# Kernel tuning notes

Measured on AMD Instinct MI355X. Metric: run time of the kernel, lower is better.

## Reference

```python
import jax, jax.numpy as jnp
import numpy as np

N = 50000      # nodes
E = 800000     # edges
DN = 128       # input node feature dim
D = 64         # dim_embed
H = 2          # attention heads (layer 0)
NEG_SLOPE = 0.2
LN_EPS = 1e-5


def setup_inputs() -> dict:
    key = jax.random.key(0)
    ks = jax.random.split(key, 10)
    s = 0.1  # weight scale
    return {
        "h":  jax.random.normal(ks[0], (N, DN), jnp.float32),
        "W0": jax.random.normal(ks[1], (DN, H * D), jnp.float32) * s,
        "al0": jax.random.normal(ks[2], (H, D), jnp.float32) * s,
        "ar0": jax.random.normal(ks[3], (H, D), jnp.float32) * s,
        "b0": jnp.zeros((H * D,), jnp.float32),
        "W1": jax.random.normal(ks[4], (H * D, D), jnp.float32) * s,
        "al1": jax.random.normal(ks[5], (1, D), jnp.float32) * s,
        "ar1": jax.random.normal(ks[6], (1, D), jnp.float32) * s,
        "b1": jnp.zeros((D,), jnp.float32),
        "g0": jnp.ones((H * D,), jnp.float32),
        "be0": jnp.zeros((H * D,), jnp.float32),
        "g1": jnp.ones((D,), jnp.float32),
        "be1": jnp.zeros((D,), jnp.float32),
        "src": jax.random.randint(ks[7], (E,), 0, N, jnp.int32),
        "dst": jax.random.randint(ks[8], (E,), 0, N, jnp.int32),
    }


def layer_norm(x, g, b):
    mu = jnp.mean(x, axis=-1, keepdims=True)
    var = jnp.mean(jnp.square(x - mu), axis=-1, keepdims=True)
    return (x - mu) * jax.lax.rsqrt(var + LN_EPS) * g + b


def gat_conv(h, W, attn_l, attn_r, bias, src, dst, heads, dim):
    # DGL GATConv (feat_drop=attn_drop=0, allow_zero_in_degree=True, bias=True)
    feat = (h @ W).reshape(-1, heads, dim)            # [N, H, D]
    el = jnp.einsum("nhd,hd->nh", feat, attn_l)       # [N, H]
    er = jnp.einsum("nhd,hd->nh", feat, attn_r)       # [N, H]
    e = jax.nn.leaky_relu(el[src] + er[dst], NEG_SLOPE)  # [E, H]
    # segment softmax over incoming edges of each dst node
    m = jax.ops.segment_max(e, dst, num_segments=N)      # [N, H]
    p = jnp.exp(e - m[dst])                              # [E, H]
    denom = jax.ops.segment_sum(p, dst, num_segments=N)  # [N, H]
    alpha = p / denom[dst]                               # [E, H]
    msg = feat[src] * alpha[:, :, None]                  # [E, H, D]
    rst = jax.ops.segment_sum(msg, dst, num_segments=N)  # [N, H, D]
    return rst + bias.reshape(1, heads, dim)


def reference(h, W0, al0, ar0, b0, W1, al1, ar1, b1, g0, be0, g1, be1, src, dst):
    # layer 0: H heads, relu(flatten), layer norm
    x = gat_conv(h, W0, al0, ar0, b0, src, dst, H, D)     # [N, H, D]
    x = jax.nn.relu(x.reshape(N, H * D))
    x = layer_norm(x, g0, be0)
    # layer 1: 1 head, mean over heads (== squeeze), layer norm
    y = gat_conv(x, W1, al1, ar1, b1, src, dst, 1, D)     # [N, 1, D]
    y = jnp.mean(y, axis=1)                               # [N, D]
    return layer_norm(y, g1, be1)
```

## Files before the change

kernel.cpp:

```cpp
#include <hip/hip_runtime.h>
#include <hip/hip_bf16.h>


#define NN 50000
#define EE 800000
#define NBUCK 196
#define CHUNK 4096
#define CAP 8192
#define GB0 ((NN + 63) / 64)

typedef _Float16 h2 __attribute__((ext_vector_type(2)));
typedef _Float16 h4 __attribute__((ext_vector_type(4)));
typedef _Float16 h8 __attribute__((ext_vector_type(8)));
typedef float f32x4 __attribute__((ext_vector_type(4)));

__device__ __forceinline__ h2 i2h(int v) { union { int i; h2 h; } u; u.i = v; return u.h; }
__device__ __forceinline__ int h2i(h2 v) { union { h2 h; int i; } u; u.h = v; return u.i; }

#define SEL_LO 0x01000504u
#define SEL_HI 0x03020706u

__global__ __launch_bounds__(1024) void k_bin(
    const int* __restrict__ src, const int* __restrict__ dst,
    int* __restrict__ bcntp, unsigned int* __restrict__ staging,
    const float* __restrict__ W0, const float* __restrict__ W1,
    h8* __restrict__ Wp0, h8* __restrict__ Wp1)
{
    int tid = threadIdx.x;
    if (blockIdx.x >= (EE + CHUNK - 1) / CHUNK) {
        int idx = (blockIdx.x - (EE + CHUNK - 1) / CHUNK) * 1024 + tid;
        if (idx < 2048) {
            int lane = idx & 63, kk = (idx >> 6) & 3, tt = idx >> 8;
            int q = lane >> 4, c = lane & 15;
            h8 v;
#pragma unroll
            for (int j = 0; j < 8; ++j)
                v[j] = (_Float16)W0[(kk * 32 + q * 8 + j) * 128 + tt * 16 + c];
            Wp0[idx] = v;
        } else if (idx < 3072) {
            int i2_ = idx - 2048;
            int lane = i2_ & 63, kk = (i2_ >> 6) & 3, tt = i2_ >> 8;
            int q = lane >> 4, c = lane & 15;
            h8 v;
#pragma unroll
            for (int j = 0; j < 8; ++j)
                v[j] = (_Float16)W1[(kk * 32 + q * 8 + j) * 64 + tt * 16 + c];
            Wp1[i2_] = v;
        }
        return;
    }
    __shared__ int hist[NBUCK];
    __shared__ int rnk[NBUCK];
    __shared__ int gbase[NBUCK];
    int base = blockIdx.x * CHUNK;
    int m = EE - base; if (m > CHUNK) m = CHUNK;
    if (tid < NBUCK) { hist[tid] = 0; rnk[tid] = 0; }
    __syncthreads();
    int e0 = tid * 4;
    bool act = e0 < m;
    int4 d4 = {0, 0, 0, 0}, s4 = {0, 0, 0, 0};
    if (act) {
        d4 = ((const int4*)(dst + base))[tid];
        s4 = ((const int4*)(src + base))[tid];
        atomicAdd(&hist[d4.x >> 8], 1);
        atomicAdd(&hist[d4.y >> 8], 1);
        atomicAdd(&hist[d4.z >> 8], 1);
        atomicAdd(&hist[d4.w >> 8], 1);
    }
    __syncthreads();
    if (tid < NBUCK && hist[tid])
        gbase[tid] = atomicAdd(&bcntp[tid * 16], hist[tid]);
    __syncthreads();
    if (act) {
        int d[4] = {d4.x, d4.y, d4.z, d4.w};
        int s[4] = {s4.x, s4.y, s4.z, s4.w};
#pragma unroll
        for (int k = 0; k < 4; ++k) {
            int b = d[k] >> 8;
            int r = atomicAdd(&rnk[b], 1);
            int slot = gbase[b] + r;
            if (slot < CAP)
                staging[(size_t)b * CAP + slot] =
                    ((unsigned)(d[k] & 255) << 16) | (unsigned)s[k];
        }
    }
}

#define HS_STRIDE 136
#define D0_STRIDE 132
__global__ __launch_bounds__(256) void k_gemm0(
    const float* __restrict__ h, const h8* __restrict__ Wp0,
    const float* __restrict__ al0, const float* __restrict__ ar0,
    _Float16* __restrict__ feat0, float* __restrict__ el0, float* __restrict__ er0,
    const int* __restrict__ bcntp, int* __restrict__ bexc, int* __restrict__ off)
{
    int tid = threadIdx.x;
    __shared__ char smem[64 * D0_STRIDE * 4];
    if (blockIdx.x == GB0) {
        int* s = (int*)smem;
        int v = (tid < NBUCK) ? bcntp[tid * 16] : 0;
        s[tid] = v;
        __syncthreads();
        for (int o = 1; o < 256; o <<= 1) {
            int u = (tid >= o) ? s[tid - o] : 0;
            __syncthreads();
            s[tid] += u;
            __syncthreads();
        }
        if (tid < NBUCK) bexc[tid] = s[tid] - v;
        if (tid == 0) off[0] = 0;
        return;
    }
    _Float16* hs = (_Float16*)smem;
    float* ds2 = (float*)smem;
    int n0 = blockIdx.x * 64;
#pragma unroll
    for (int r = 0; r < 8; ++r) {
        int f = tid + 256 * r;
        int node = f >> 5, kc = f & 31;
        int n = n0 + node;
        float4 v = {0.f, 0.f, 0.f, 0.f};
        if (n < NN) v = ((const float4*)h)[(size_t)n * 32 + kc];
        h4 hv; hv[0] = (_Float16)v.x; hv[1] = (_Float16)v.y;
        hv[2] = (_Float16)v.z; hv[3] = (_Float16)v.w;
        *(h4*)&hs[node * HS_STRIDE + kc * 4] = hv;
    }
    __syncthreads();
    int w = tid >> 6, lane = tid & 63;
    int m = lane & 15, q = lane >> 4;
    h8 aF[4];
#pragma unroll
    for (int kk = 0; kk < 4; ++kk)
        aF[kk] = *(const h8*)&hs[(w * 16 + m) * HS_STRIDE + kk * 32 + q * 8];
    __syncthreads();
#pragma unroll
    for (int t = 0; t < 8; ++t) {
        f32x4 acc = {0.f, 0.f, 0.f, 0.f};
#pragma unroll
        for (int kk = 0; kk < 4; ++kk) {
            h8 bF = Wp0[(t * 4 + kk) * 64 + lane];
            acc = __builtin_amdgcn_mfma_f32_16x16x32_f16(aF[kk], bF, acc, 0, 0, 0);
        }
#pragma unroll
        for (int r = 0; r < 4; ++r)
            ds2[(w * 16 + q * 4 + r) * D0_STRIDE + t * 16 + m] = acc[r];
    }
    __syncthreads();
#pragma unroll
    for (int r = 0; r < 4; ++r) {
        int f = tid + 256 * r;
        int node = f >> 4, c8 = f & 15;
        int n = n0 + node;
        if (n < NN) {
            float4 a = *(const float4*)&ds2[node * D0_STRIDE + c8 * 8];
            float4 b = *(const float4*)&ds2[node * D0_STRIDE + c8 * 8 + 4];
            h8 v;
            v[0] = (_Float16)a.x; v[1] = (_Float16)a.y; v[2] = (_Float16)a.z; v[3] = (_Float16)a.w;
            v[4] = (_Float16)b.x; v[5] = (_Float16)b.y; v[6] = (_Float16)b.z; v[7] = (_Float16)b.w;
            ((h8*)feat0)[(size_t)n * 16 + c8] = v;
        }
    }
    {
        int node = tid >> 2, qq = tid & 3;
        int n = n0 + node;
        float pl = 0.f, pr = 0.f;
#pragma unroll
        for (int i = 0; i < 8; ++i) {
            float4 v = *(const float4*)&ds2[node * D0_STRIDE + qq * 32 + i * 4];
            float4 a = ((const float4*)al0)[qq * 8 + i];
            float4 r = ((const float4*)ar0)[qq * 8 + i];
            pl += v.x * a.x + v.y * a.y + v.z * a.z + v.w * a.w;
            pr += v.x * r.x + v.y * r.y + v.z * r.z + v.w * r.w;
        }
        pl += __shfl_xor(pl, 1, 4); pr += __shfl_xor(pr, 1, 4);
        if (n < NN) {
            if (qq == 0) { el0[n * 2] = pl;     er0[n * 2] = pr; }
            if (qq == 2) { el0[n * 2 + 1] = pl; er0[n * 2 + 1] = pr; }
        }
    }
}

__global__ __launch_bounds__(256) void k_final(
    const unsigned int* __restrict__ staging, const int* __restrict__ bcntp,
    const int* __restrict__ bexc, int* __restrict__ off,
    unsigned short* __restrict__ ssort)
{
    int b = blockIdx.x;
    int tid = threadIdx.x;
    int cnt = bcntp[b * 16]; if (cnt > CAP) cnt = CAP;
    size_t base = (size_t)b * CAP;
    int lo = bexc[b];
    __shared__ unsigned short buf[CAP];
    __shared__ int hist[256];
    __shared__ int sc[256];
    hist[tid] = 0;
    __syncthreads();
    for (int i = tid; i < cnt; i += 256)
        atomicAdd(&hist[staging[base + i] >> 16], 1);
    __syncthreads();
    int hv = hist[tid];
    sc[tid] = hv;
    __syncthreads();
    for (int o = 1; o < 256; o <<= 1) {
        int u = (tid >= o) ? sc[tid - o] : 0;
        __syncthreads();
        sc[tid] += u;
        __syncthreads();
    }
    int nlo = b << 8;
    int nrem = NN - nlo; if (nrem > 256) nrem = 256;
    if (tid < nrem) off[nlo + tid + 1] = lo + sc[tid];
    hist[tid] = sc[tid] - hv;
    __syncthreads();
    for (int i = tid; i < cnt; i += 256) {
        unsigned rec = staging[base + i];
        int r = atomicAdd(&hist[rec >> 16], 1);
        buf[r] = (unsigned short)(rec & 0xFFFFu);
    }
    __syncthreads();
    for (int i = tid; i < cnt; i += 256)
        ssort[lo + i] = buf[i];
}

#define D1_STRIDE 68
__global__ __launch_bounds__(1024) void k_aggemm(
    const int* __restrict__ off, const unsigned short* __restrict__ ssort,
    const float* __restrict__ el0, const float* __restrict__ er0,
    const _Float16* __restrict__ feat0, const float* __restrict__ b0,
    const float* __restrict__ g0, const float* __restrict__ be0,
    const h8* __restrict__ Wp1, const float* __restrict__ al1,
    const float* __restrict__ ar1,
    _Float16* __restrict__ feat1, float* __restrict__ el1, float* __restrict__ er1)
{
    int tid = threadIdx.x;
    int w16 = tid >> 6, lane = tid & 63;
    int grp = lane >> 4, c = lane & 15;
    int n0 = blockIdx.x * 64;
    __shared__ char smem[64 * HS_STRIDE * 2 > 64 * D1_STRIDE * 4
                         ? 64 * HS_STRIDE * 2 : 64 * D1_STRIDE * 4];
    __shared__ int2 esc[16][64];
    _Float16* xs = (_Float16*)smem;
    float* ds2 = (float*)smem;
    const int4* fb = (const int4*)feat0;
    unsigned qsel = (c < 8) ? SEL_LO : SEL_HI;
    for (int i = 0; i < 4; ++i) {
        int nl = w16 * 4 + i;
        int n = n0 + nl;
        if (n < NN) {
            int beg = off[n], end = off[n + 1];
            float2 ern2 = ((const float2*)er0)[n];
            float acc[8] = {};
            float den0 = 0.f, den1 = 0.f;
            for (int cb = beg; cb < end; cb += 64) {
                int m = end - cb; if (m > 64) m = 64;
                int s_reg = 0; float p0 = 0.f, p1 = 0.f;
                if (lane < m) {
                    s_reg = ssort[cb + lane];
                    float2 el2 = ((const float2*)el0)[s_reg];
                    float v0 = el2.x + ern2.x; v0 = v0 > 0.f ? v0 : 0.2f * v0;
                    float v1 = el2.y + ern2.y; v1 = v1 > 0.f ? v1 : 0.2f * v1;
                    p0 = __expf(v0); p1 = __expf(v1);
                }
                den0 += p0; den1 += p1;
                h2 pp; pp[0] = (_Float16)p0; pp[1] = (_Float16)p1;
                esc[w16][lane] = make_int2(s_reg, h2i(pp));
                for (int ii = 0; ii < m; ii += 8) {
                    int4 rr = *(const int4*)&esc[w16][ii + grp * 2];
                    int qp = __builtin_amdgcn_perm(rr.y, rr.w, qsel);
                    int4 iA = fb[(size_t)rr.x * 16 + c];
                    int4 iB = fb[(size_t)rr.z * 16 + c];
                    h2 q2 = i2h(qp);
                    int pe, po;
                    pe = __builtin_amdgcn_perm(iA.x, iB.x, SEL_LO);
                    po = __builtin_amdgcn_perm(iA.x, iB.x, SEL_HI);
                    acc[0] = __builtin_amdgcn_fdot2(i2h(pe), q2, acc[0], false);
                    acc[1] = __builtin_amdgcn_fdot2(i2h(po), q2, acc[1], false);
                    pe = __builtin_amdgcn_perm(iA.y, iB.y, SEL_LO);
                    po = __builtin_amdgcn_perm(iA.y, iB.y, SEL_HI);
                    acc[2] = __builtin_amdgcn_fdot2(i2h(pe), q2, acc[2], false);
                    acc[3] = __builtin_amdgcn_fdot2(i2h(po), q2, acc[3], false);
                    pe = __builtin_amdgcn_perm(iA.z, iB.z, SEL_LO);
                    po = __builtin_amdgcn_perm(iA.z, iB.z, SEL_HI);
                    acc[4] = __builtin_amdgcn_fdot2(i2h(pe), q2, acc[4], false);
                    acc[5] = __builtin_amdgcn_fdot2(i2h(po), q2, acc[5], false);
                    pe = __builtin_amdgcn_perm(iA.w, iB.w, SEL_LO);
                    po = __builtin_amdgcn_perm(iA.w, iB.w, SEL_HI);
                    acc[6] = __builtin_amdgcn_fdot2(i2h(pe), q2, acc[6], false);
                    acc[7] = __builtin_amdgcn_fdot2(i2h(po), q2, acc[7], false);
                }
            }
#pragma unroll
            for (int k = 0; k < 8; ++k) {
                acc[k] += __shfl_down(acc[k], 32);
                acc[k] += __shfl_down(acc[k], 16);
            }
#pragma unroll
            for (int o = 32; o > 0; o >>= 1) { den0 += __shfl_down(den0, o); den1 += __shfl_down(den1, o); }
            den0 = __shfl(den0, 0); den1 = __shfl(den1, 0);
            float den = (c < 8) ? den0 : den1;
            float inv = (end > beg) ? 1.f / den : 0.f;
            float4 ba = ((const float4*)b0)[c * 2];
            float4 bb = ((const float4*)b0)[c * 2 + 1];
            float val[8];
            val[0] = fmaxf(acc[0] * inv + ba.x, 0.f);
            val[1] = fmaxf(acc[1] * inv + ba.y, 0.f);
            val[2] = fmaxf(acc[2] * inv + ba.z, 0.f);
            val[3] = fmaxf(acc[3] * inv + ba.w, 0.f);
            val[4] = fmaxf(acc[4] * inv + bb.x, 0.f);
            val[5] = fmaxf(acc[5] * inv + bb.y, 0.f);
            val[6] = fmaxf(acc[6] * inv + bb.z, 0.f);
            val[7] = fmaxf(acc[7] * inv + bb.w, 0.f);
            float s1 = 0.f, s2 = 0.f;
#pragma unroll
            for (int k = 0; k < 8; ++k) { s1 += val[k]; s2 += val[k] * val[k]; }
#pragma unroll
            for (int o = 1; o < 16; o <<= 1) { s1 += __shfl_xor(s1, o, 16); s2 += __shfl_xor(s2, o, 16); }
            float mu = s1 * (1.f / 128.f);
            float var = s2 * (1.f / 128.f) - mu * mu;
            float rs = rsqrtf(var + 1e-5f);
            if (grp == 0) {
                float4 ga = ((const float4*)g0)[c * 2];
                float4 gb = ((const float4*)g0)[c * 2 + 1];
                float4 ea = ((const float4*)be0)[c * 2];
                float4 eb = ((const float4*)be0)[c * 2 + 1];
                h8 xv;
                xv[0] = (_Float16)((val[0] - mu) * rs * ga.x + ea.x);
                xv[1] = (_Float16)((val[1] - mu) * rs * ga.y + ea.y);
                xv[2] = (_Float16)((val[2] - mu) * rs * ga.z + ea.z);
                xv[3] = (_Float16)((val[3] - mu) * rs * ga.w + ea.w);
                xv[4] = (_Float16)((val[4] - mu) * rs * gb.x + eb.x);
                xv[5] = (_Float16)((val[5] - mu) * rs * gb.y + eb.y);
                xv[6] = (_Float16)((val[6] - mu) * rs * gb.z + eb.z);
                xv[7] = (_Float16)((val[7] - mu) * rs * gb.w + eb.w);
                *(h8*)&xs[nl * HS_STRIDE + c * 8] = xv;
            }
        } else if (grp == 0) {
            h8 z = {};
            *(h8*)&xs[nl * HS_STRIDE + c * 8] = z;
        }
    }
    __syncthreads();
    int rg = w16 & 3, t = w16 >> 2;
    int m = lane & 15, q = lane >> 4;
    h8 aF[4];
#pragma unroll
    for (int kk = 0; kk < 4; ++kk)
        aF[kk] = *(const h8*)&xs[(rg * 16 + m) * HS_STRIDE + kk * 32 + q * 8];
    __syncthreads();
    f32x4 acc1 = {0.f, 0.f, 0.f, 0.f};
#pragma unroll
    for (int kk = 0; kk < 4; ++kk) {
        h8 bF = Wp1[(t * 4 + kk) * 64 + lane];
        acc1 = __builtin_amdgcn_mfma_f32_16x16x32_f16(aF[kk], bF, acc1, 0, 0, 0);
    }
#pragma unroll
    for (int r = 0; r < 4; ++r)
        ds2[(rg * 16 + q * 4 + r) * D1_STRIDE + t * 16 + m] = acc1[r];
    __syncthreads();
    if (tid < 512) {
        int node = tid >> 3, c8 = tid & 7;
        int n = n0 + node;
        if (n < NN) {
            float4 a = *(const float4*)&ds2[node * D1_STRIDE + c8 * 8];
            float4 b = *(const float4*)&ds2[node * D1_STRIDE + c8 * 8 + 4];
            h8 v;
            v[0] = (_Float16)a.x; v[1] = (_Float16)a.y; v[2] = (_Float16)a.z; v[3] = (_Float16)a.w;
            v[4] = (_Float16)b.x; v[5] = (_Float16)b.y; v[6] = (_Float16)b.z; v[7] = (_Float16)b.w;
            ((h8*)feat1)[(size_t)n * 8 + c8] = v;
        }
    } else if (tid < 768) {
        int t2 = tid - 512;
        int node = t2 >> 2, qq = t2 & 3;
        int n = n0 + node;
        float pl = 0.f, pr = 0.f;
#pragma unroll
        for (int i = 0; i < 4; ++i) {
            float4 v = *(const float4*)&ds2[node * D1_STRIDE + qq * 16 + i * 4];
            float4 a = ((const float4*)al1)[qq * 4 + i];
            float4 r = ((const float4*)ar1)[qq * 4 + i];
            pl += v.x * a.x + v.y * a.y + v.z * a.z + v.w * a.w;
            pr += v.x * r.x + v.y * r.y + v.z * r.z + v.w * r.w;
        }
        pl += __shfl_xor(pl, 1, 4); pr += __shfl_xor(pr, 1, 4);
        pl += __shfl_xor(pl, 2, 4); pr += __shfl_xor(pr, 2, 4);
        if (qq == 0 && n < NN) { el1[n] = pl; er1[n] = pr; }
    }
}

__global__ __launch_bounds__(256) void k_agg1(
    const int* __restrict__ off, const unsigned short* __restrict__ ssort,
    const float* __restrict__ el1, const float* __restrict__ er1,
    const _Float16* __restrict__ feat1, const float* __restrict__ b1,
    const float* __restrict__ g1, const float* __restrict__ be1,
    float* __restrict__ out)
{
    int w = threadIdx.x >> 6, lane = threadIdx.x & 63;
    int grp = lane >> 3, c = lane & 7;
    int n = blockIdx.x * 4 + w;
    int beg = off[n], end = off[n + 1];
    float ern = er1[n];
    const int4* fb = (const int4*)feat1;
    __shared__ int2 esc[4][64];
    float acc[8] = {};
    float den = 0.f;
    for (int cb = beg; cb < end; cb += 64) {
        int m = end - cb; if (m > 64) m = 64;
        int s_reg = 0; float p_reg = 0.f;
        if (lane < m) {
            s_reg = ssort[cb + lane];
            float v = el1[s_reg] + ern;
            v = v > 0.f ? v : 0.2f * v;
            p_reg = __expf(v);
        }
        den += p_reg;
        h2 pp; pp[0] = (_Float16)p_reg; pp[1] = (_Float16)0.f;
        esc[w][lane] = make_int2(s_reg, h2i(pp));
        for (int i = 0; i < m; i += 16) {
            int4 rr = *(const int4*)&esc[w][i + grp * 2];
            int qp = __builtin_amdgcn_perm(rr.y, rr.w, SEL_LO);
            int4 iA = fb[(size_t)rr.x * 8 + c];
            int4 iB = fb[(size_t)rr.z * 8 + c];
            h2 q2 = i2h(qp);
            int pe, po;
            pe = __builtin_amdgcn_perm(iA.x, iB.x, SEL_LO);
            po = __builtin_amdgcn_perm(iA.x, iB.x, SEL_HI);
            acc[0] = __builtin_amdgcn_fdot2(i2h(pe), q2, acc[0], false);
            acc[1] = __builtin_amdgcn_fdot2(i2h(po), q2, acc[1], false);
            pe = __builtin_amdgcn_perm(iA.y, iB.y, SEL_LO);
            po = __builtin_amdgcn_perm(iA.y, iB.y, SEL_HI);
            acc[2] = __builtin_amdgcn_fdot2(i2h(pe), q2, acc[2], false);
            acc[3] = __builtin_amdgcn_fdot2(i2h(po), q2, acc[3], false);
            pe = __builtin_amdgcn_perm(iA.z, iB.z, SEL_LO);
            po = __builtin_amdgcn_perm(iA.z, iB.z, SEL_HI);
            acc[4] = __builtin_amdgcn_fdot2(i2h(pe), q2, acc[4], false);
            acc[5] = __builtin_amdgcn_fdot2(i2h(po), q2, acc[5], false);
            pe = __builtin_amdgcn_perm(iA.w, iB.w, SEL_LO);
            po = __builtin_amdgcn_perm(iA.w, iB.w, SEL_HI);
            acc[6] = __builtin_amdgcn_fdot2(i2h(pe), q2, acc[6], false);
            acc[7] = __builtin_amdgcn_fdot2(i2h(po), q2, acc[7], false);
        }
    }
#pragma unroll
    for (int k = 0; k < 8; ++k) {
        acc[k] += __shfl_down(acc[k], 32);
        acc[k] += __shfl_down(acc[k], 16);
        acc[k] += __shfl_down(acc[k], 8);
    }
#pragma unroll
    for (int o = 32; o > 0; o >>= 1) den += __shfl_down(den, o);
    den = __shfl(den, 0);
    float inv = (end > beg) ? 1.f / den : 0.f;
    float4 ba = ((const float4*)b1)[c * 2];
    float4 bb = ((const float4*)b1)[c * 2 + 1];
    float val[8];
    val[0] = acc[0] * inv + ba.x; val[1] = acc[1] * inv + ba.y;
    val[2] = acc[2] * inv + ba.z; val[3] = acc[3] * inv + ba.w;
    val[4] = acc[4] * inv + bb.x; val[5] = acc[5] * inv + bb.y;
    val[6] = acc[6] * inv + bb.z; val[7] = acc[7] * inv + bb.w;
    float s1 = 0.f, s2 = 0.f;
#pragma unroll
    for (int k = 0; k < 8; ++k) { s1 += val[k]; s2 += val[k] * val[k]; }
#pragma unroll
    for (int o = 1; o < 8; o <<= 1) { s1 += __shfl_xor(s1, o, 8); s2 += __shfl_xor(s2, o, 8); }
    float mu = s1 * (1.f / 64.f);
    float var = s2 * (1.f / 64.f) - mu * mu;
    float rs = rsqrtf(var + 1e-5f);
    if (lane < 8) {
        float4 ga = ((const float4*)g1)[c * 2];
        float4 gb = ((const float4*)g1)[c * 2 + 1];
        float4 ea = ((const float4*)be1)[c * 2];
        float4 eb = ((const float4*)be1)[c * 2 + 1];
        float4 oa, ob;
        oa.x = (val[0] - mu) * rs * ga.x + ea.x;
        oa.y = (val[1] - mu) * rs * ga.y + ea.y;
        oa.z = (val[2] - mu) * rs * ga.z + ea.z;
        oa.w = (val[3] - mu) * rs * ga.w + ea.w;
        ob.x = (val[4] - mu) * rs * gb.x + eb.x;
        ob.y = (val[5] - mu) * rs * gb.y + eb.y;
        ob.z = (val[6] - mu) * rs * gb.z + eb.z;
        ob.w = (val[7] - mu) * rs * gb.w + eb.w;
        float4* orow = (float4*)(out + (size_t)n * 64);
        orow[c * 2] = oa;
        orow[c * 2 + 1] = ob;
    }
}

extern "C" void kernel_launch(void* const* d_in, const int* in_sizes, int n_in,
                              void* d_out, int out_size, void* d_ws, size_t ws_size,
                              hipStream_t stream)
{
    const float* h   = (const float*)d_in[0];
    const float* W0  = (const float*)d_in[1];
    const float* al0 = (const float*)d_in[2];
    const float* ar0 = (const float*)d_in[3];
    const float* b0  = (const float*)d_in[4];
    const float* W1  = (const float*)d_in[5];
    const float* al1 = (const float*)d_in[6];
    const float* ar1 = (const float*)d_in[7];
    const float* b1  = (const float*)d_in[8];
    const float* g0  = (const float*)d_in[9];
    const float* be0 = (const float*)d_in[10];
    const float* g1  = (const float*)d_in[11];
    const float* be1 = (const float*)d_in[12];
    const int*   src = (const int*)d_in[13];
    const int*   dst = (const int*)d_in[14];
    float* out = (float*)d_out;

    char* p = (char*)d_ws;
    auto alloc = [&](size_t bytes) -> char* {
        char* r = p;
        p += (bytes + 255) & ~(size_t)255;
        return r;
    };
    _Float16* feat0 = (_Float16*)alloc((size_t)NN * 128 * sizeof(_Float16));
    float* el0   = (float*)alloc((size_t)NN * 2 * sizeof(float));
    float* er0   = (float*)alloc((size_t)NN * 2 * sizeof(float));
    _Float16* feat1 = (_Float16*)alloc((size_t)NN * 64 * sizeof(_Float16));
    float* el1   = (float*)alloc((size_t)NN * sizeof(float));
    float* er1   = (float*)alloc((size_t)NN * sizeof(float));
    int*   bcntp = (int*)alloc((size_t)NBUCK * 16 * sizeof(int));
    int*   bexc  = (int*)alloc((size_t)NBUCK * sizeof(int));
    int*   off   = (int*)alloc((size_t)(NN + 1) * sizeof(int));
    unsigned int*   staging = (unsigned int*)alloc((size_t)NBUCK * CAP * sizeof(unsigned int));
    unsigned short* ssort   = (unsigned short*)alloc((size_t)EE * sizeof(unsigned short));
    h8*    Wp0   = (h8*)alloc(2048 * sizeof(h8));
    h8*    Wp1   = (h8*)alloc(1024 * sizeof(h8));

    hipMemsetAsync(bcntp, 0, (size_t)NBUCK * 16 * sizeof(int), stream);

    const int NBBIN = (EE + CHUNK - 1) / CHUNK;
    k_bin<<<NBBIN + 3, 1024, 0, stream>>>(src, dst, bcntp, staging, W0, W1, Wp0, Wp1);
    k_gemm0<<<GB0 + 1, 256, 0, stream>>>(h, Wp0, al0, ar0, feat0, el0, er0,
                                         bcntp, bexc, off);
    k_final<<<NBUCK, 256, 0, stream>>>(staging, bcntp, bexc, off, ssort);
    k_aggemm<<<(NN + 63) / 64, 1024, 0, stream>>>(off, ssort, el0, er0, feat0,
                                                  b0, g0, be0, Wp1, al1, ar1,
                                                  feat1, el1, er1);
    k_agg1<<<NN / 4, 256, 0, stream>>>(off, ssort, el1, er1, feat1, b1, g1, be1, out);
}
```

Measured before the change: 208.8 us.

## Fuse binning with layer-0 GEMM, move bucket scan into sort, remap aggregation lanes per node

Replaces the memset and weight-packing prologue with a small init kernel, and merges edge binning with the layer-0 GEMM into one 1024-thread launch. The bucket prefix scan moves into each k_final block, which removes the bexc buffer. Both aggregation kernels now assign one node per 16-lane (layer 0) or 8-lane (layer 1) group instead of one node per wavefront. This drops the cross-lane accumulator reductions and raises occupancy for the low-degree nodes. The cost is redundant scans across blocks and less memory-level parallelism on high-degree nodes.

```diff
diff --git a/kernel.cpp b/kernel.cpp
--- a/kernel.cpp
+++ b/kernel.cpp
@@ -7,7 +7,7 @@
 #define NBUCK 196
 #define CHUNK 4096
 #define CAP 8192
-#define GB0 ((NN + 63) / 64)
+#define NBBIN 196
 
 typedef _Float16 h2 __attribute__((ext_vector_type(2)));
 typedef _Float16 h4 __attribute__((ext_vector_type(4)));
@@ -20,103 +20,90 @@
 #define SEL_LO 0x01000504u
 #define SEL_HI 0x03020706u
 
-__global__ __launch_bounds__(1024) void k_bin(
+__global__ __launch_bounds__(1024) void k_init(
+    const float* __restrict__ W0, const float* __restrict__ W1,
+    h8* __restrict__ Wp0, h8* __restrict__ Wp1, int* __restrict__ bcntp)
+{
+    int tid = threadIdx.x;
+    int b = blockIdx.x;
+    if (b < 2) {
+        int idx = b * 1024 + tid;
+        int lane = idx & 63, kk = (idx >> 6) & 3, tt = idx >> 8;
+        int q = lane >> 4, c = lane & 15;
+        h8 v;
+#pragma unroll
+        for (int j = 0; j < 8; ++j)
+            v[j] = (_Float16)W0[(kk * 32 + q * 8 + j) * 128 + tt * 16 + c];
+        Wp0[idx] = v;
+    } else if (b == 2) {
+        int idx = tid;
+        int lane = idx & 63, kk = (idx >> 6) & 3, tt = idx >> 8;
+        int q = lane >> 4, c = lane & 15;
+        h8 v;
+#pragma unroll
+        for (int j = 0; j < 8; ++j)
+            v[j] = (_Float16)W1[(kk * 32 + q * 8 + j) * 64 + tt * 16 + c];
+        Wp1[idx] = v;
+    } else {
+        for (int i = tid; i < NBUCK * 16; i += 1024) bcntp[i] = 0;
+    }
+}
+
+#define HS_STRIDE 136
+#define D0_STRIDE 132
+__global__ __launch_bounds__(1024) void k_work(
     const int* __restrict__ src, const int* __restrict__ dst,
     int* __restrict__ bcntp, unsigned int* __restrict__ staging,
-    const float* __restrict__ W0, const float* __restrict__ W1,
-    h8* __restrict__ Wp0, h8* __restrict__ Wp1)
+    const float* __restrict__ h, const h8* __restrict__ Wp0,
+    const float* __restrict__ al0, const float* __restrict__ ar0,
+    _Float16* __restrict__ feat0, float* __restrict__ el0, float* __restrict__ er0)
 {
     int tid = threadIdx.x;
-    if (blockIdx.x >= (EE + CHUNK - 1) / CHUNK) {
-        int idx = (blockIdx.x - (EE + CHUNK - 1) / CHUNK) * 1024 + tid;
-        if (idx < 2048) {
-            int lane = idx & 63, kk = (idx >> 6) & 3, tt = idx >> 8;
-            int q = lane >> 4, c = lane & 15;
-            h8 v;
-#pragma unroll
-            for (int j = 0; j < 8; ++j)
-                v[j] = (_Float16)W0[(kk * 32 + q * 8 + j) * 128 + tt * 16 + c];
-            Wp0[idx] = v;
-        } else if (idx < 3072) {
-            int i2_ = idx - 2048;
-            int lane = i2_ & 63, kk = (i2_ >> 6) & 3, tt = i2_ >> 8;
-            int q = lane >> 4, c = lane & 15;
-            h8 v;
-#pragma unroll
-            for (int j = 0; j < 8; ++j)
-                v[j] = (_Float16)W1[(kk * 32 + q * 8 + j) * 64 + tt * 16 + c];
-            Wp1[i2_] = v;
-        }
-        return;
-    }
+    __shared__ char smem[64 * D0_STRIDE * 4];
     __shared__ int hist[NBUCK];
     __shared__ int rnk[NBUCK];
     __shared__ int gbase[NBUCK];
-    int base = blockIdx.x * CHUNK;
-    int m = EE - base; if (m > CHUNK) m = CHUNK;
-    if (tid < NBUCK) { hist[tid] = 0; rnk[tid] = 0; }
-    __syncthreads();
-    int e0 = tid * 4;
-    bool act = e0 < m;
-    int4 d4 = {0, 0, 0, 0}, s4 = {0, 0, 0, 0};
-    if (act) {
-        d4 = ((const int4*)(dst + base))[tid];
-        s4 = ((const int4*)(src + base))[tid];
-        atomicAdd(&hist[d4.x >> 8], 1);
-        atomicAdd(&hist[d4.y >> 8], 1);
-        atomicAdd(&hist[d4.z >> 8], 1);
-        atomicAdd(&hist[d4.w >> 8], 1);
-    }
-    __syncthreads();
-    if (tid < NBUCK && hist[tid])
-        gbase[tid] = atomicAdd(&bcntp[tid * 16], hist[tid]);
-    __syncthreads();
-    if (act) {
-        int d[4] = {d4.x, d4.y, d4.z, d4.w};
-        int s[4] = {s4.x, s4.y, s4.z, s4.w};
-#pragma unroll
-        for (int k = 0; k < 4; ++k) {
-            int b = d[k] >> 8;
-            int r = atomicAdd(&rnk[b], 1);
-            int slot = gbase[b] + r;
-            if (slot < CAP)
-                staging[(size_t)b * CAP + slot] =
-                    ((unsigned)(d[k] & 255) << 16) | (unsigned)s[k];
-        }
-    }
-}
-
-#define HS_STRIDE 136
-#define D0_STRIDE 132
-__global__ __launch_bounds__(256) void k_gemm0(
-    const float* __restrict__ h, const h8* __restrict__ Wp0,
-    const float* __restrict__ al0, const float* __restrict__ ar0,
-    _Float16* __restrict__ feat0, float* __restrict__ el0, float* __restrict__ er0,
-    const int* __restrict__ bcntp, int* __restrict__ bexc, int* __restrict__ off)
-{
-    int tid = threadIdx.x;
-    __shared__ char smem[64 * D0_STRIDE * 4];
-    if (blockIdx.x == GB0) {
-        int* s = (int*)smem;
-        int v = (tid < NBUCK) ? bcntp[tid * 16] : 0;
-        s[tid] = v;
-        __syncthreads();
-        for (int o = 1; o < 256; o <<= 1) {
-            int u = (tid >= o) ? s[tid - o] : 0;
-            __syncthreads();
-            s[tid] += u;
-            __syncthreads();
-        }
-        if (tid < NBUCK) bexc[tid] = s[tid] - v;
-        if (tid == 0) off[0] = 0;
+    if (blockIdx.x < NBBIN) {
+        int base = blockIdx.x * CHUNK;
+        int m = EE - base; if (m > CHUNK) m = CHUNK;
+        if (tid < NBUCK) { hist[tid] = 0; rnk[tid] = 0; }
+        __syncthreads();
+        int e0 = tid * 4;
+        bool act = e0 < m;
+        int4 d4 = {0, 0, 0, 0}, s4 = {0, 0, 0, 0};
+        if (act) {
+            d4 = ((const int4*)(dst + base))[tid];
+            s4 = ((const int4*)(src + base))[tid];
+            atomicAdd(&hist[d4.x >> 8], 1);
+            atomicAdd(&hist[d4.y >> 8], 1);
+            atomicAdd(&hist[d4.z >> 8], 1);
+            atomicAdd(&hist[d4.w >> 8], 1);
+        }
+        __syncthreads();
+        if (tid < NBUCK && hist[tid])
+            gbase[tid] = atomicAdd(&bcntp[tid * 16], hist[tid]);
+        __syncthreads();
+        if (act) {
+            int d[4] = {d4.x, d4.y, d4.z, d4.w};
+            int s[4] = {s4.x, s4.y, s4.z, s4.w};
+#pragma unroll
+            for (int k = 0; k < 4; ++k) {
+                int b = d[k] >> 8;
+                int r = atomicAdd(&rnk[b], 1);
+                int slot = gbase[b] + r;
+                if (slot < CAP)
+                    staging[(size_t)b * CAP + slot] =
+                        ((unsigned)(d[k] & 255) << 16) | (unsigned)s[k];
+            }
+        }
         return;
     }
     _Float16* hs = (_Float16*)smem;
     float* ds2 = (float*)smem;
-    int n0 = blockIdx.x * 64;
-#pragma unroll
-    for (int r = 0; r < 8; ++r) {
-        int f = tid + 256 * r;
+    int n0 = (blockIdx.x - NBBIN) * 64;
+#pragma unroll
+    for (int r = 0; r < 2; ++r) {
+        int f = tid + 1024 * r;
         int node = f >> 5, kc = f & 31;
         int n = n0 + node;
         float4 v = {0.f, 0.f, 0.f, 0.f};
@@ -126,15 +113,17 @@
         *(h4*)&hs[node * HS_STRIDE + kc * 4] = hv;
     }
     __syncthreads();
-    int w = tid >> 6, lane = tid & 63;
+    int w16 = tid >> 6, lane = tid & 63;
+    int rg = w16 & 3, tt = w16 >> 2;
     int m = lane & 15, q = lane >> 4;
     h8 aF[4];
 #pragma unroll
     for (int kk = 0; kk < 4; ++kk)
-        aF[kk] = *(const h8*)&hs[(w * 16 + m) * HS_STRIDE + kk * 32 + q * 8];
-    __syncthreads();
-#pragma unroll
-    for (int t = 0; t < 8; ++t) {
+        aF[kk] = *(const h8*)&hs[(rg * 16 + m) * HS_STRIDE + kk * 32 + q * 8];
+    __syncthreads();
+#pragma unroll
+    for (int t2 = 0; t2 < 2; ++t2) {
+        int t = tt * 2 + t2;
         f32x4 acc = {0.f, 0.f, 0.f, 0.f};
 #pragma unroll
         for (int kk = 0; kk < 4; ++kk) {
@@ -143,13 +132,11 @@
         }
 #pragma unroll
         for (int r = 0; r < 4; ++r)
-            ds2[(w * 16 + q * 4 + r) * D0_STRIDE + t * 16 + m] = acc[r];
-    }
-    __syncthreads();
-#pragma unroll
-    for (int r = 0; r < 4; ++r) {
-        int f = tid + 256 * r;
-        int node = f >> 4, c8 = f & 15;
+            ds2[(rg * 16 + q * 4 + r) * D0_STRIDE + t * 16 + m] = acc[r];
+    }
+    __syncthreads();
+    {
+        int node = tid >> 4, c8 = tid & 15;
         int n = n0 + node;
         if (n < NN) {
             float4 a = *(const float4*)&ds2[node * D0_STRIDE + c8 * 8];
@@ -160,7 +147,7 @@
             ((h8*)feat0)[(size_t)n * 16 + c8] = v;
         }
     }
-    {
+    if (tid < 256) {
         int node = tid >> 2, qq = tid & 3;
         int n = n0 + node;
         float pl = 0.f, pr = 0.f;
@@ -182,17 +169,27 @@
 
 __global__ __launch_bounds__(256) void k_final(
     const unsigned int* __restrict__ staging, const int* __restrict__ bcntp,
-    const int* __restrict__ bexc, int* __restrict__ off,
-    unsigned short* __restrict__ ssort)
+    int* __restrict__ off, unsigned short* __restrict__ ssort)
 {
     int b = blockIdx.x;
     int tid = threadIdx.x;
     int cnt = bcntp[b * 16]; if (cnt > CAP) cnt = CAP;
     size_t base = (size_t)b * CAP;
-    int lo = bexc[b];
     __shared__ unsigned short buf[CAP];
     __shared__ int hist[256];
     __shared__ int sc[256];
+    int bv = (tid < NBUCK) ? bcntp[tid * 16] : 0;
+    sc[tid] = bv;
+    __syncthreads();
+    for (int o = 1; o < 256; o <<= 1) {
+        int u = (tid >= o) ? sc[tid - o] : 0;
+        __syncthreads();
+        sc[tid] += u;
+        __syncthreads();
+    }
+    int lo = (b > 0) ? sc[b - 1] : 0;
+    if (b == 0 && tid == 0) off[0] = 0;
+    __syncthreads();
     hist[tid] = 0;
     __syncthreads();
     for (int i = tid; i < cnt; i += 256)
@@ -234,28 +231,28 @@
 {
     int tid = threadIdx.x;
     int w16 = tid >> 6, lane = tid & 63;
-    int grp = lane >> 4, c = lane & 15;
+    int g = lane >> 4, c = lane & 15;
     int n0 = blockIdx.x * 64;
     __shared__ char smem[64 * HS_STRIDE * 2 > 64 * D1_STRIDE * 4
                          ? 64 * HS_STRIDE * 2 : 64 * D1_STRIDE * 4];
-    __shared__ int2 esc[16][64];
+    __shared__ int2 esc[16][4][18];
     _Float16* xs = (_Float16*)smem;
     float* ds2 = (float*)smem;
     const int4* fb = (const int4*)feat0;
     unsigned qsel = (c < 8) ? SEL_LO : SEL_HI;
-    for (int i = 0; i < 4; ++i) {
-        int nl = w16 * 4 + i;
+    {
+        int nl = w16 * 4 + g;
         int n = n0 + nl;
         if (n < NN) {
             int beg = off[n], end = off[n + 1];
             float2 ern2 = ((const float2*)er0)[n];
             float acc[8] = {};
             float den0 = 0.f, den1 = 0.f;
-            for (int cb = beg; cb < end; cb += 64) {
-                int m = end - cb; if (m > 64) m = 64;
+            for (int cb = beg; cb < end; cb += 16) {
+                int m = end - cb; if (m > 16) m = 16;
                 int s_reg = 0; float p0 = 0.f, p1 = 0.f;
-                if (lane < m) {
-                    s_reg = ssort[cb + lane];
+                if (c < m) {
+                    s_reg = ssort[cb + c];
                     float2 el2 = ((const float2*)el0)[s_reg];
                     float v0 = el2.x + ern2.x; v0 = v0 > 0.f ? v0 : 0.2f * v0;
                     float v1 = el2.y + ern2.y; v1 = v1 > 0.f ? v1 : 0.2f * v1;
@@ -263,9 +260,9 @@
                 }
                 den0 += p0; den1 += p1;
                 h2 pp; pp[0] = (_Float16)p0; pp[1] = (_Float16)p1;
-                esc[w16][lane] = make_int2(s_reg, h2i(pp));
-                for (int ii = 0; ii < m; ii += 8) {
-                    int4 rr = *(const int4*)&esc[w16][ii + grp * 2];
+                esc[w16][g][c] = make_int2(s_reg, h2i(pp));
+                for (int ii = 0; ii < m; ii += 2) {
+                    int4 rr = *(const int4*)&esc[w16][g][ii];
                     int qp = __builtin_amdgcn_perm(rr.y, rr.w, qsel);
                     int4 iA = fb[(size_t)rr.x * 16 + c];
                     int4 iB = fb[(size_t)rr.z * 16 + c];
@@ -290,13 +287,10 @@
                 }
             }
 #pragma unroll
-            for (int k = 0; k < 8; ++k) {
-                acc[k] += __shfl_down(acc[k], 32);
-                acc[k] += __shfl_down(acc[k], 16);
+            for (int o = 1; o < 16; o <<= 1) {
+                den0 += __shfl_xor(den0, o, 16);
+                den1 += __shfl_xor(den1, o, 16);
             }
-#pragma unroll
-            for (int o = 32; o > 0; o >>= 1) { den0 += __shfl_down(den0, o); den1 += __shfl_down(den1, o); }
-            den0 = __shfl(den0, 0); den1 = __shfl(den1, 0);
             float den = (c < 8) ? den0 : den1;
             float inv = (end > beg) ? 1.f / den : 0.f;
             float4 ba = ((const float4*)b0)[c * 2];
@@ -318,23 +312,21 @@
             float mu = s1 * (1.f / 128.f);
             float var = s2 * (1.f / 128.f) - mu * mu;
             float rs = rsqrtf(var + 1e-5f);
-            if (grp == 0) {
-                float4 ga = ((const float4*)g0)[c * 2];
-                float4 gb = ((const float4*)g0)[c * 2 + 1];
-                float4 ea = ((const float4*)be0)[c * 2];
-                float4 eb = ((const float4*)be0)[c * 2 + 1];
-                h8 xv;
-                xv[0] = (_Float16)((val[0] - mu) * rs * ga.x + ea.x);
-                xv[1] = (_Float16)((val[1] - mu) * rs * ga.y + ea.y);
-                xv[2] = (_Float16)((val[2] - mu) * rs * ga.z + ea.z);
-                xv[3] = (_Float16)((val[3] - mu) * rs * ga.w + ea.w);
-                xv[4] = (_Float16)((val[4] - mu) * rs * gb.x + eb.x);
-                xv[5] = (_Float16)((val[5] - mu) * rs * gb.y + eb.y);
-                xv[6] = (_Float16)((val[6] - mu) * rs * gb.z + eb.z);
-                xv[7] = (_Float16)((val[7] - mu) * rs * gb.w + eb.w);
-                *(h8*)&xs[nl * HS_STRIDE + c * 8] = xv;
-            }
-        } else if (grp == 0) {
+            float4 ga = ((const float4*)g0)[c * 2];
+            float4 gb = ((const float4*)g0)[c * 2 + 1];
+            float4 ea = ((const float4*)be0)[c * 2];
+            float4 eb = ((const float4*)be0)[c * 2 + 1];
+            h8 xv;
+            xv[0] = (_Float16)((val[0] - mu) * rs * ga.x + ea.x);
+            xv[1] = (_Float16)((val[1] - mu) * rs * ga.y + ea.y);
+            xv[2] = (_Float16)((val[2] - mu) * rs * ga.z + ea.z);
+            xv[3] = (_Float16)((val[3] - mu) * rs * ga.w + ea.w);
+            xv[4] = (_Float16)((val[4] - mu) * rs * gb.x + eb.x);
+            xv[5] = (_Float16)((val[5] - mu) * rs * gb.y + eb.y);
+            xv[6] = (_Float16)((val[6] - mu) * rs * gb.z + eb.z);
+            xv[7] = (_Float16)((val[7] - mu) * rs * gb.w + eb.w);
+            *(h8*)&xs[nl * HS_STRIDE + c * 8] = xv;
+        } else {
             h8 z = {};
             *(h8*)&xs[nl * HS_STRIDE + c * 8] = z;
         }
@@ -395,28 +387,29 @@
     float* __restrict__ out)
 {
     int w = threadIdx.x >> 6, lane = threadIdx.x & 63;
-    int grp = lane >> 3, c = lane & 7;
-    int n = blockIdx.x * 4 + w;
+    int g = lane >> 3, c = lane & 7;
+    int n = blockIdx.x * 32 + w * 8 + g;
+    __shared__ int2 esc[4][8][10];
+    const int4* fb = (const int4*)feat1;
+    if (n >= NN) return;
     int beg = off[n], end = off[n + 1];
     float ern = er1[n];
-    const int4* fb = (const int4*)feat1;
-    __shared__ int2 esc[4][64];
     float acc[8] = {};
     float den = 0.f;
-    for (int cb = beg; cb < end; cb += 64) {
-        int m = end - cb; if (m > 64) m = 64;
+    for (int cb = beg; cb < end; cb += 8) {
+        int m = end - cb; if (m > 8) m = 8;
         int s_reg = 0; float p_reg = 0.f;
-        if (lane < m) {
-            s_reg = ssort[cb + lane];
+        if (c < m) {
+            s_reg = ssort[cb + c];
             float v = el1[s_reg] + ern;
             v = v > 0.f ? v : 0.2f * v;
             p_reg = __expf(v);
         }
         den += p_reg;
         h2 pp; pp[0] = (_Float16)p_reg; pp[1] = (_Float16)0.f;
-        esc[w][lane] = make_int2(s_reg, h2i(pp));
-        for (int i = 0; i < m; i += 16) {
-            int4 rr = *(const int4*)&esc[w][i + grp * 2];
+        esc[w][g][c] = make_int2(s_reg, h2i(pp));
+        for (int ii = 0; ii < m; ii += 2) {
+            int4 rr = *(const int4*)&esc[w][g][ii];
             int qp = __builtin_amdgcn_perm(rr.y, rr.w, SEL_LO);
             int4 iA = fb[(size_t)rr.x * 8 + c];
             int4 iB = fb[(size_t)rr.z * 8 + c];
@@ -441,14 +434,7 @@
         }
     }
 #pragma unroll
-    for (int k = 0; k < 8; ++k) {
-        acc[k] += __shfl_down(acc[k], 32);
-        acc[k] += __shfl_down(acc[k], 16);
-        acc[k] += __shfl_down(acc[k], 8);
-    }
-#pragma unroll
-    for (int o = 32; o > 0; o >>= 1) den += __shfl_down(den, o);
-    den = __shfl(den, 0);
+    for (int o = 1; o < 8; o <<= 1) den += __shfl_xor(den, o, 8);
     float inv = (end > beg) ? 1.f / den : 0.f;
     float4 ba = ((const float4*)b1)[c * 2];
     float4 bb = ((const float4*)b1)[c * 2 + 1];
@@ -465,24 +451,22 @@
     float mu = s1 * (1.f / 64.f);
     float var = s2 * (1.f / 64.f) - mu * mu;
     float rs = rsqrtf(var + 1e-5f);
-    if (lane < 8) {
-        float4 ga = ((const float4*)g1)[c * 2];
-        float4 gb = ((const float4*)g1)[c * 2 + 1];
-        float4 ea = ((const float4*)be1)[c * 2];
-        float4 eb = ((const float4*)be1)[c * 2 + 1];
-        float4 oa, ob;
-        oa.x = (val[0] - mu) * rs * ga.x + ea.x;
-        oa.y = (val[1] - mu) * rs * ga.y + ea.y;
-        oa.z = (val[2] - mu) * rs * ga.z + ea.z;
-        oa.w = (val[3] - mu) * rs * ga.w + ea.w;
-        ob.x = (val[4] - mu) * rs * gb.x + eb.x;
-        ob.y = (val[5] - mu) * rs * gb.y + eb.y;
-        ob.z = (val[6] - mu) * rs * gb.z + eb.z;
-        ob.w = (val[7] - mu) * rs * gb.w + eb.w;
-        float4* orow = (float4*)(out + (size_t)n * 64);
-        orow[c * 2] = oa;
-        orow[c * 2 + 1] = ob;
-    }
+    float4 ga = ((const float4*)g1)[c * 2];
+    float4 gb = ((const float4*)g1)[c * 2 + 1];
+    float4 ea = ((const float4*)be1)[c * 2];
+    float4 eb = ((const float4*)be1)[c * 2 + 1];
+    float4 oa, ob;
+    oa.x = (val[0] - mu) * rs * ga.x + ea.x;
+    oa.y = (val[1] - mu) * rs * ga.y + ea.y;
+    oa.z = (val[2] - mu) * rs * ga.z + ea.z;
+    oa.w = (val[3] - mu) * rs * ga.w + ea.w;
+    ob.x = (val[4] - mu) * rs * gb.x + eb.x;
+    ob.y = (val[5] - mu) * rs * gb.y + eb.y;
+    ob.z = (val[6] - mu) * rs * gb.z + eb.z;
+    ob.w = (val[7] - mu) * rs * gb.w + eb.w;
+    float4* orow = (float4*)(out + (size_t)n * 64);
+    orow[c * 2] = oa;
+    orow[c * 2 + 1] = ob;
 }
 
 extern "C" void kernel_launch(void* const* d_in, const int* in_sizes, int n_in,
@@ -519,22 +503,20 @@
     float* el1   = (float*)alloc((size_t)NN * sizeof(float));
     float* er1   = (float*)alloc((size_t)NN * sizeof(float));
     int*   bcntp = (int*)alloc((size_t)NBUCK * 16 * sizeof(int));
-    int*   bexc  = (int*)alloc((size_t)NBUCK * sizeof(int));
     int*   off   = (int*)alloc((size_t)(NN + 1) * sizeof(int));
     unsigned int*   staging = (unsigned int*)alloc((size_t)NBUCK * CAP * sizeof(unsigned int));
     unsigned short* ssort   = (unsigned short*)alloc((size_t)EE * sizeof(unsigned short));
     h8*    Wp0   = (h8*)alloc(2048 * sizeof(h8));
     h8*    Wp1   = (h8*)alloc(1024 * sizeof(h8));
 
-    hipMemsetAsync(bcntp, 0, (size_t)NBUCK * 16 * sizeof(int), stream);
-
-    const int NBBIN = (EE + CHUNK - 1) / CHUNK;
-    k_bin<<<NBBIN + 3, 1024, 0, stream>>>(src, dst, bcntp, staging, W0, W1, Wp0, Wp1);
-    k_gemm0<<<GB0 + 1, 256, 0, stream>>>(h, Wp0, al0, ar0, feat0, el0, er0,
-                                         bcntp, bexc, off);
-    k_final<<<NBUCK, 256, 0, stream>>>(staging, bcntp, bexc, off, ssort);
+    const int GB0 = (NN + 63) / 64;
+    k_init<<<4, 1024, 0, stream>>>(W0, W1, Wp0, Wp1, bcntp);
+    k_work<<<NBBIN + GB0, 1024, 0, stream>>>(src, dst, bcntp, staging,
+                                             h, Wp0, al0, ar0, feat0, el0, er0);
+    k_final<<<NBUCK, 256, 0, stream>>>(staging, bcntp, off, ssort);
     k_aggemm<<<(NN + 63) / 64, 1024, 0, stream>>>(off, ssort, el0, er0, feat0,
                                                   b0, g0, be0, Wp1, al1, ar1,
                                                   feat1, el1, er1);
-    k_agg1<<<NN / 4, 256, 0, stream>>>(off, ssort, el1, er1, feat1, b1, g1, be1, out);
+    k_agg1<<<(NN + 31) / 32, 256, 0, stream>>>(off, ssort, el1, er1, feat1,
+                                               b1, g1, be1, out);
 }
```

After: 187.2 us. 10.3% less time.
